# Kernel tuning notes

Hardware: AMD Instinct MI355X
Metric: run time of the kernel (lower is better)

Reference implementation:

```python
import jax, jax.numpy as jnp
import numpy as np

DIMS = 1024
BATCH, SEQ = 4, 2048

def setup_inputs() -> dict:
    key = jax.random.key(0)
    k1, k2, k3, k4 = jax.random.split(key, 4)
    scale = 1.0 / np.sqrt(DIMS)
    return {
        "input_seq_embs": jax.random.normal(k1, (BATCH, SEQ, DIMS), dtype=jnp.float32),
        "Wq": jax.random.normal(k2, (DIMS, DIMS), dtype=jnp.float32) * scale,
        "Wk": jax.random.normal(k3, (DIMS, DIMS), dtype=jnp.float32) * scale,
        "Wv": jax.random.normal(k4, (DIMS, DIMS), dtype=jnp.float32) * scale,
    }

def reference(input_seq_embs, Wq, Wk, Wv):
    # nn.Linear(x) = x @ W.T ; weights stored [out, in]
    q = jnp.einsum('bsd,ed->bse', input_seq_embs, Wq)
    k = jnp.einsum('bsd,ed->bse', input_seq_embs, Wk)
    v = jnp.einsum('bsd,ed->bse', input_seq_embs, Wv)
    # full N x N scores, NO 1/sqrt(d) scaling (faithful to source)
    scores = jnp.einsum('bqe,bke->bqk', q, k)
    causal = jnp.tril(jnp.ones((q.shape[1], q.shape[1]), dtype=bool))
    scores = jnp.where(causal[None, :, :], scores, -jnp.inf)
    attn = jax.nn.softmax(scores, axis=-1)
    return jnp.einsum('bqk,bke->bqe', attn, v)
```

## Files before the change

### kernel.cpp

```cpp
#include <hip/hip_runtime.h>


typedef _Float16 h8 __attribute__((ext_vector_type(8)));
typedef float f32x4 __attribute__((ext_vector_type(4)));

#define BM 128
#define BN 128
#define BK 32

__device__ __forceinline__ void gl_lds16(const _Float16* g, _Float16* l) {
    __builtin_amdgcn_global_load_lds(
        (const __attribute__((address_space(1))) void*)g,
        (__attribute__((address_space(3))) void*)l, 16, 0, 0);
}

template<bool OUT_F16, bool TRI, bool KLIM>
__global__ __launch_bounds__(256) void gemm_nt(
    const _Float16* __restrict__ A, const _Float16* __restrict__ B,
    void* __restrict__ Cp, int N, int K,
    size_t sAz, size_t sBz, size_t sCz)
{
    __shared__ _Float16 As[BM * BK];
    __shared__ _Float16 Bs[BN * BK];

    int bx, by;
    if (TRI) {
        const int t = blockIdx.x;
        int i = (int)((sqrtf((float)(8 * t + 1)) - 1.0f) * 0.5f);
        while ((i + 1) * (i + 2) / 2 <= t) i++;
        while (i * (i + 1) / 2 > t) i--;
        by = i;
        bx = t - i * (i + 1) / 2;
    } else {
        bx = blockIdx.x;
        by = blockIdx.y;
    }

    const int tid  = threadIdx.x;
    const int lane = tid & 63;
    const int wv   = tid >> 6;
    const int m0 = by * BM, n0 = bx * BN;
    const size_t z = blockIdx.z;

    const int lr = lane >> 2;
    const int lc = (lane & 3) * 8;
    const _Float16* pA0 = A + z * sAz + (size_t)(m0 + wv * 16 + lr) * K + lc;
    const _Float16* pA1 = pA0 + (size_t)64 * K;
    const _Float16* pB0 = B + z * sBz + (size_t)(n0 + wv * 16 + lr) * K + lc;
    const _Float16* pB1 = pB0 + (size_t)64 * K;
    _Float16* lA0 = As + wv * 512;
    _Float16* lA1 = As + (wv + 4) * 512;
    _Float16* lB0 = Bs + wv * 512;
    _Float16* lB1 = Bs + (wv + 4) * 512;

    const int la = lane & 15;
    const int qd = lane >> 4;
    const int wm = (wv >> 1) * 64;
    const int wn = (wv & 1) * 64;

    f32x4 acc[4][4];
    #pragma unroll
    for (int i = 0; i < 4; i++)
        #pragma unroll
        for (int j = 0; j < 4; j++)
            acc[i][j] = (f32x4){0.f, 0.f, 0.f, 0.f};

    const int kEnd = KLIM ? (m0 + BM) : K;

    for (int k0 = 0; k0 < kEnd; k0 += BK) {
        gl_lds16(pA0, lA0);
        gl_lds16(pA1, lA1);
        gl_lds16(pB0, lB0);
        gl_lds16(pB1, lB1);
        pA0 += BK; pA1 += BK; pB0 += BK; pB1 += BK;
        __syncthreads();

        h8 af[4], bf[4];
        #pragma unroll
        for (int i = 0; i < 4; i++)
            af[i] = *(const h8*)&As[(wm + i * 16 + la) * BK + qd * 8];
        #pragma unroll
        for (int i = 0; i < 4; i++)
            bf[i] = *(const h8*)&Bs[(wn + i * 16 + la) * BK + qd * 8];
        #pragma unroll
        for (int i = 0; i < 4; i++)
            #pragma unroll
            for (int j = 0; j < 4; j++)
                acc[i][j] = __builtin_amdgcn_mfma_f32_16x16x32_f16(af[i], bf[j], acc[i][j], 0, 0, 0);
        __syncthreads();
    }

    if (OUT_F16) {
        _Float16* C = (_Float16*)Cp + z * sCz;
        #pragma unroll
        for (int i = 0; i < 4; i++)
            #pragma unroll
            for (int j = 0; j < 4; j++)
                #pragma unroll
                for (int rr = 0; rr < 4; rr++)
                    C[(size_t)(m0 + wm + i * 16 + qd * 4 + rr) * N + (n0 + wn + j * 16 + la)] =
                        (_Float16)acc[i][j][rr];
    } else {
        float* C = (float*)Cp + z * sCz;
        #pragma unroll
        for (int i = 0; i < 4; i++)
            #pragma unroll
            for (int j = 0; j < 4; j++)
                #pragma unroll
                for (int rr = 0; rr < 4; rr++)
                    C[(size_t)(m0 + wm + i * 16 + qd * 4 + rr) * N + (n0 + wn + j * 16 + la)] =
                        acc[i][j][rr];
    }
}

__global__ __launch_bounds__(256) void cvt8(const float* __restrict__ in,
                                            _Float16* __restrict__ out)
{
    const size_t i = ((size_t)blockIdx.x * 256 + threadIdx.x) * 8;
    float4 a = *(const float4*)(in + i);
    float4 b = *(const float4*)(in + i + 4);
    h8 o = { (_Float16)a.x, (_Float16)a.y, (_Float16)a.z, (_Float16)a.w,
             (_Float16)b.x, (_Float16)b.y, (_Float16)b.z, (_Float16)b.w };
    *(h8*)(out + i) = o;
}

__global__ __launch_bounds__(256) void cvt_w3(const float* __restrict__ Wq,
                                              const float* __restrict__ Wk,
                                              const float* __restrict__ Wv,
                                              _Float16* __restrict__ out)
{
    const int zz = blockIdx.y;
    const float* in = (zz == 0) ? Wq : ((zz == 1) ? Wk : Wv);
    const size_t i = ((size_t)blockIdx.x * 256 + threadIdx.x) * 8;
    float4 a = *(const float4*)(in + i);
    float4 b = *(const float4*)(in + i + 4);
    h8 o = { (_Float16)a.x, (_Float16)a.y, (_Float16)a.z, (_Float16)a.w,
             (_Float16)b.x, (_Float16)b.y, (_Float16)b.z, (_Float16)b.w };
    *(h8*)(out + (size_t)zz * 1048576 + i) = o;
}

__global__ __launch_bounds__(256) void softmax_causal(const float* __restrict__ S,
                                                      _Float16* __restrict__ P)
{
    const int idx = blockIdx.x;
    const int q = idx & 2047;
    const float* Srow = S + (size_t)idx * 2048;
    _Float16* Prow = P + (size_t)idx * 2048;
    const int t = threadIdx.x;
    const int lane = t & 63, wv = t >> 6;
    __shared__ float red[4];

    float vals[8];
    float mx = -3.4e38f;
    #pragma unroll
    for (int i = 0; i < 8; i++) {
        int k = t + i * 256;
        float v = (k <= q) ? Srow[k] : -3.4e38f;
        vals[i] = v;
        mx = fmaxf(mx, v);
    }
    #pragma unroll
    for (int o = 32; o > 0; o >>= 1) mx = fmaxf(mx, __shfl_down(mx, o, 64));
    if (lane == 0) red[wv] = mx;
    __syncthreads();
    const float mall = fmaxf(fmaxf(red[0], red[1]), fmaxf(red[2], red[3]));
    __syncthreads();

    float sum = 0.f;
    #pragma unroll
    for (int i = 0; i < 8; i++) {
        int k = t + i * 256;
        float e = (k <= q) ? __expf(vals[i] - mall) : 0.f;
        vals[i] = e;
        sum += e;
    }
    #pragma unroll
    for (int o = 32; o > 0; o >>= 1) sum += __shfl_down(sum, o, 64);
    if (lane == 0) red[wv] = sum;
    __syncthreads();
    const float inv = 1.f / (red[0] + red[1] + red[2] + red[3]);

    #pragma unroll
    for (int i = 0; i < 8; i++)
        Prow[t + i * 256] = (_Float16)(vals[i] * inv);
}

__global__ __launch_bounds__(256) void transpose_v_kernel(const _Float16* __restrict__ V,
                                                          _Float16* __restrict__ Vt)
{
    __shared__ _Float16 tile[64][72];
    const int b = blockIdx.z;
    const int s0 = blockIdx.x * 64;
    const int e0 = blockIdx.y * 64;
    const _Float16* Vb = V + (size_t)b * 2048 * 1024;
    _Float16* Vtb = Vt + (size_t)b * 1024 * 2048;
    const int r = threadIdx.x >> 2;
    const int c = (threadIdx.x & 3) * 16;

    const _Float16* src = &Vb[(size_t)(s0 + r) * 1024 + e0 + c];
    *(uint4*)&tile[r][c]     = *(const uint4*)src;
    *(uint4*)&tile[r][c + 8] = *(const uint4*)(src + 8);
    __syncthreads();

    h8 o0, o1;
    #pragma unroll
    for (int j = 0; j < 8; j++) o0[j] = tile[c + j][r];
    #pragma unroll
    for (int j = 0; j < 8; j++) o1[j] = tile[c + 8 + j][r];
    _Float16* dst = &Vtb[(size_t)(e0 + r) * 2048 + s0 + c];
    *(h8*)dst       = o0;
    *(h8*)(dst + 8) = o1;
}

extern "C" void kernel_launch(void* const* d_in, const int* in_sizes, int n_in,
                              void* d_out, int out_size, void* d_ws, size_t ws_size,
                              hipStream_t stream) {
    const float* x  = (const float*)d_in[0];
    const float* Wq = (const float*)d_in[1];
    const float* Wk = (const float*)d_in[2];
    const float* Wv = (const float*)d_in[3];
    float* out = (float*)d_out;

    const size_t MiB = 1024 * 1024;
    char* ws = (char*)d_ws;
    _Float16* QKVh = (_Float16*)ws;
    _Float16* Vh   = QKVh + (size_t)2 * 8388608;
    float*    S    = (float*)(ws + 48 * MiB);
    _Float16* x_h  = (_Float16*)(ws + 48 * MiB);
    _Float16* Wh   = (_Float16*)(ws + 64 * MiB);
    _Float16* P    = (_Float16*)ws;
    _Float16* Vt   = (_Float16*)(ws + 48 * MiB);

    const dim3 blk(256);

    cvt8<<<dim3(4096), blk, 0, stream>>>(x, x_h);
    cvt_w3<<<dim3(512, 3), blk, 0, stream>>>(Wq, Wk, Wv, Wh);

    gemm_nt<true, false, false><<<dim3(8, 64, 3), blk, 0, stream>>>(
        x_h, Wh, QKVh, 1024, 1024,
        (size_t)0, (size_t)1048576, (size_t)8388608);

    gemm_nt<false, true, false><<<dim3(136, 1, 4), blk, 0, stream>>>(
        QKVh, QKVh + 8388608, S, 2048, 1024,
        (size_t)2097152, (size_t)2097152, (size_t)4194304);

    softmax_causal<<<dim3(4 * 2048), blk, 0, stream>>>(S, P);

    transpose_v_kernel<<<dim3(32, 16, 4), blk, 0, stream>>>(Vh, Vt);

    gemm_nt<false, false, true><<<dim3(8, 16, 4), blk, 0, stream>>>(
        P, Vt, out, 1024, 2048,
        (size_t)4194304, (size_t)2097152, (size_t)2097152);
}
```

Baseline: 290.1 us.

## Fuse QKV projections, swizzle GEMM block order, and trim masked softmax work

The three projection GEMMs become one GEMM with N=3072 over the concatenated weights. Its epilogue scatters each column range into the separate Q, K and V buffers. New block-index swizzles group tiles for L2 reuse in the projection. They also replace the sqrt-based triangular index decode in QK^T and pair short and long causal rows in PV for load balance. Softmax now skips loads and exps for fully masked chunks and stores P only up to the 128-aligned causal bound that the PV GEMM actually reads, which relies on that GEMM's K limit.

```diff
diff --git a/kernel.cpp b/kernel.cpp
--- a/kernel.cpp
+++ b/kernel.cpp
@@ -14,7 +14,7 @@
         (__attribute__((address_space(3))) void*)l, 16, 0, 0);
 }
 
-template<bool OUT_F16, bool TRI, bool KLIM>
+template<int SWZ, int OM, bool KLIM>
 __global__ __launch_bounds__(256) void gemm_nt(
     const _Float16* __restrict__ A, const _Float16* __restrict__ B,
     void* __restrict__ Cp, int N, int K,
@@ -24,16 +24,20 @@
     __shared__ _Float16 Bs[BN * BK];
 
     int bx, by;
-    if (TRI) {
-        const int t = blockIdx.x;
-        int i = (int)((sqrtf((float)(8 * t + 1)) - 1.0f) * 0.5f);
-        while ((i + 1) * (i + 2) / 2 <= t) i++;
-        while (i * (i + 1) / 2 > t) i--;
-        by = i;
-        bx = t - i * (i + 1) / 2;
+    if (SWZ == 1) {
+        const int r = blockIdx.x & 7, q2 = blockIdx.x >> 3;
+        bx = q2 >> 3;
+        by = ((q2 & 7) << 3) | r;
+    } else if (SWZ == 2) {
+        const int r = blockIdx.x & 7, g = blockIdx.x >> 3;
+        if (g <= r) { by = r;      bx = g; }
+        else        { by = 15 - r; bx = g - (r + 1); }
+    } else if (SWZ == 3) {
+        const int r = blockIdx.x & 7, g = blockIdx.x >> 3;
+        by = (g & 1) ? (15 - r) : r;
+        bx = g >> 1;
     } else {
-        bx = blockIdx.x;
-        by = blockIdx.y;
+        bx = blockIdx.x; by = blockIdx.y;
     }
 
     const int tid  = threadIdx.x;
@@ -90,7 +94,20 @@
         __syncthreads();
     }
 
-    if (OUT_F16) {
+    if (OM == 2) {
+        _Float16* C = (_Float16*)Cp;
+        #pragma unroll
+        for (int i = 0; i < 4; i++)
+            #pragma unroll
+            for (int j = 0; j < 4; j++) {
+                const int col  = n0 + wn + j * 16 + la;
+                const size_t base = (size_t)(col >> 10) * 8388608 + (col & 1023);
+                #pragma unroll
+                for (int rr = 0; rr < 4; rr++)
+                    C[base + (size_t)(m0 + wm + i * 16 + qd * 4 + rr) * 1024] =
+                        (_Float16)acc[i][j][rr];
+            }
+    } else if (OM == 1) {
         _Float16* C = (_Float16*)Cp + z * sCz;
         #pragma unroll
         for (int i = 0; i < 4; i++)
@@ -154,10 +171,12 @@
     float mx = -3.4e38f;
     #pragma unroll
     for (int i = 0; i < 8; i++) {
-        int k = t + i * 256;
-        float v = (k <= q) ? Srow[k] : -3.4e38f;
-        vals[i] = v;
-        mx = fmaxf(mx, v);
+        vals[i] = -3.4e38f;
+        if (i * 256 <= q) {
+            int k = t + i * 256;
+            if (k <= q) vals[i] = Srow[k];
+            mx = fmaxf(mx, vals[i]);
+        }
     }
     #pragma unroll
     for (int o = 32; o > 0; o >>= 1) mx = fmaxf(mx, __shfl_down(mx, o, 64));
@@ -169,10 +188,12 @@
     float sum = 0.f;
     #pragma unroll
     for (int i = 0; i < 8; i++) {
-        int k = t + i * 256;
-        float e = (k <= q) ? __expf(vals[i] - mall) : 0.f;
-        vals[i] = e;
-        sum += e;
+        if (i * 256 <= q) {
+            int k = t + i * 256;
+            float e = (k <= q) ? __expf(vals[i] - mall) : 0.f;
+            vals[i] = e;
+            sum += e;
+        } else vals[i] = 0.f;
     }
     #pragma unroll
     for (int o = 32; o > 0; o >>= 1) sum += __shfl_down(sum, o, 64);
@@ -180,9 +201,13 @@
     __syncthreads();
     const float inv = 1.f / (red[0] + red[1] + red[2] + red[3]);
 
-    #pragma unroll
-    for (int i = 0; i < 8; i++)
-        Prow[t + i * 256] = (_Float16)(vals[i] * inv);
+    const int kceil = ((q >> 7) + 1) << 7;
+    #pragma unroll
+    for (int i = 0; i < 8; i++) {
+        if (i * 256 >= kceil) break;
+        int k = t + i * 256;
+        if (k < kceil) Prow[k] = (_Float16)(vals[i] * inv);
+    }
 }
 
 __global__ __launch_bounds__(256) void transpose_v_kernel(const _Float16* __restrict__ V,
@@ -236,11 +261,10 @@
     cvt8<<<dim3(4096), blk, 0, stream>>>(x, x_h);
     cvt_w3<<<dim3(512, 3), blk, 0, stream>>>(Wq, Wk, Wv, Wh);
 
-    gemm_nt<true, false, false><<<dim3(8, 64, 3), blk, 0, stream>>>(
-        x_h, Wh, QKVh, 1024, 1024,
-        (size_t)0, (size_t)1048576, (size_t)8388608);
-
-    gemm_nt<false, true, false><<<dim3(136, 1, 4), blk, 0, stream>>>(
+    gemm_nt<1, 2, false><<<dim3(1536), blk, 0, stream>>>(
+        x_h, Wh, QKVh, 3072, 1024, 0, 0, 0);
+
+    gemm_nt<2, 0, false><<<dim3(136, 1, 4), blk, 0, stream>>>(
         QKVh, QKVh + 8388608, S, 2048, 1024,
         (size_t)2097152, (size_t)2097152, (size_t)4194304);
 
@@ -248,7 +272,7 @@
 
     transpose_v_kernel<<<dim3(32, 16, 4), blk, 0, stream>>>(Vh, Vt);
 
-    gemm_nt<false, false, true><<<dim3(8, 16, 4), blk, 0, stream>>>(
+    gemm_nt<3, 0, true><<<dim3(128, 1, 4), blk, 0, stream>>>(
         P, Vt, out, 1024, 2048,
         (size_t)4194304, (size_t)2097152, (size_t)2097152);
 }
```

New measurement: 283.3 us. -2.4%, faster.
